# Optimization experiments

Measured on AMD Instinct MI355X. Metric: run time of the kernel, lower is better.

Reference implementation:

```python
import jax, jax.numpy as jnp
import numpy as np

E = 8      # num_experts
D = 1024   # input_size
H = 1024   # hidden_size
K = 2      # top_k
B = 2
S = 1024


def setup_inputs() -> dict:
    key = jax.random.key(0)
    ks = jax.random.split(key, 5)
    x = jax.random.normal(ks[0], (B, S, D), dtype=jnp.float32)
    p = jax.random.uniform(ks[1], (B * S, K), dtype=jnp.float32)
    expert_p = p / p.sum(axis=-1, keepdims=True)            # normalized top-k gates
    expert_idxs = jax.random.randint(ks[2], (B * S, K), 0, E)
    W1 = jax.random.normal(ks[3], (E, D, 2 * H), dtype=jnp.float32) * (D ** -0.5)
    W2 = jax.random.normal(ks[4], (E, H, D), dtype=jnp.float32) * (H ** -0.5)
    return {"x": x, "expert_p": expert_p, "expert_idxs": expert_idxs, "W1": W1, "W2": W2}


def reference(x, expert_p, expert_idxs, W1, W2):
    x_shape = x.shape
    xf = x.reshape(-1, x_shape[-1])                 # [N, D]
    n_tok = xf.shape[0]
    k = expert_idxs.shape[-1]
    x_pair = jnp.repeat(xf, k, axis=0)              # [N*K, D] token replicated per expert slot
    idx = expert_idxs.reshape(-1)                   # [N*K]
    p = expert_p.reshape(-1)                        # [N*K]
    y_pair = jnp.zeros((n_tok * k, x_shape[-1]), dtype=x.dtype)
    # loop over fixed small expert count; masked dense GEMM per expert
    for e in range(W1.shape[0]):
        m = (idx == e).astype(x.dtype)[:, None]     # [N*K, 1]
        hg = (x_pair * m) @ W1[e]                   # [N*K, 2H]
        h, g = jnp.split(hg, 2, axis=-1)            # chunk(2): (h, gates)
        a = jax.nn.silu(g) * h                      # SiLU-gated GLU
        y_pair = y_pair + (a @ W2[e]) * m           # [N*K, D]
    # combine: weight each pair by its gate prob and sum over top_k slots
    y = (y_pair * p[:, None]).reshape(n_tok, k, -1).sum(axis=1)
    return y.reshape(x_shape)
```

## Files before the change

kernel.cpp:

```cpp
#include <hip/hip_runtime.h>


typedef __bf16 bf16x8 __attribute__((ext_vector_type(8)));
typedef __bf16 bf16x4 __attribute__((ext_vector_type(4)));
typedef float  f32x4  __attribute__((ext_vector_type(4)));

#define NPAIR 4096
#define NTOK  2048
#define DDIM  1024
#define HDIM  1024
#define NEXP  8

#define ORDER_I   64
#define XB_OFF    (24576)
#define W1T_OFF   (XB_OFF + 4194304)
#define W2T_OFF   (W1T_OFF + 33554432)
#define ACT_OFF   (W2T_OFF + 16777216)

#define GLOAD_LDS16(g, l) \
    __builtin_amdgcn_global_load_lds( \
        (const __attribute__((address_space(1))) void*)(g), \
        (__attribute__((address_space(3))) void*)(l), 16, 0, 0)

__device__ __forceinline__ void tcvt64(const float* __restrict__ s,
                                       __bf16* __restrict__ d,
                                       int R, int C, int k0, int c0,
                                       float (*tt)[65], int tid) {
#pragma unroll
    for (int p = 0; p < 4; p++) {
        int kr = p * 16 + (tid >> 4);
        int nc = (tid & 15) * 4;
        *(float4*)&tt[kr][nc] = *(const float4*)(s + (size_t)(k0 + kr) * C + c0 + nc);
    }
    __syncthreads();
#pragma unroll
    for (int p = 0; p < 2; p++) {
        int cid = p * 256 + tid;
        int n = cid >> 3, kc = cid & 7;
        bf16x8 o;
#pragma unroll
        for (int j = 0; j < 8; j++) o[j] = (__bf16)tt[kc * 8 + j][n];
        *(bf16x8*)(d + (size_t)(c0 + n) * R + k0 + kc * 8) = o;
    }
}

__global__ __launch_bounds__(256) void prep_kernel(const float* __restrict__ x,
                                                   const float* __restrict__ W1,
                                                   const int* __restrict__ idx,
                                                   int* __restrict__ wsi,
                                                   __bf16* __restrict__ xb,
                                                   __bf16* __restrict__ w1t) {
    __shared__ float tt[64][65];
    __shared__ int cnt[NEXP];
    __shared__ int sbase, scur;
    const int b = blockIdx.x;
    const int tid = threadIdx.x;
    if (b < 4096) {
        int e = b >> 9, t2 = b & 511;
        int k0 = (t2 & 15) * 64, c0 = (t2 >> 4) * 64;
        tcvt64(W1 + (size_t)e * DDIM * 2 * HDIM, w1t + (size_t)e * 2 * HDIM * DDIM,
               DDIM, 2 * HDIM, k0, c0, tt, tid);
    } else if (b < 6144) {
        int i = (b - 4096) * 1024 + tid * 4;
        float4 v = *(const float4*)(x + i);
        bf16x4 o;
        o[0] = (__bf16)v.x; o[1] = (__bf16)v.y; o[2] = (__bf16)v.z; o[3] = (__bf16)v.w;
        *(bf16x4*)(xb + i) = o;
    } else {
        const int e = b - 6144;
        if (tid < NEXP) cnt[tid] = 0;
        if (tid == 0) scur = 0;
        __syncthreads();
        for (int i = tid; i < NPAIR; i += 256) atomicAdd(&cnt[idx[i] & 7], 1);
        __syncthreads();
        if (tid == 0) {
            int off = 0;
            for (int e2 = 0; e2 < NEXP; e2++) {
                if (e2 == e) { wsi[e] = cnt[e]; wsi[8 + e] = off; sbase = off; }
                off += (cnt[e2] + 127) & ~127;
            }
        }
        __syncthreads();
        for (int i = tid; i < NPAIR; i += 256) {
            if ((idx[i] & 7) == e) {
                int s = atomicAdd(&scur, 1);
                wsi[ORDER_I + sbase + s] = i;
            }
        }
    }
}

__global__ __launch_bounds__(256) void gemm1_kernel(const __bf16* __restrict__ xb,
                                                    const __bf16* __restrict__ w1t,
                                                    const int* __restrict__ wsi,
                                                    __bf16* __restrict__ act,
                                                    const float* __restrict__ W2,
                                                    __bf16* __restrict__ w2t,
                                                    float* __restrict__ out) {
    __shared__ __align__(16) char smem[24576];
    const int tid = threadIdx.x;
    const int z = blockIdx.z;

    if (z >= 8) {
        int aux = (z - 8) * 1024 + blockIdx.y * 16 + blockIdx.x;
        if (aux < 2048) {
            int e = aux >> 8, t2 = aux & 255;
            int k0 = (t2 & 15) * 64, c0 = (t2 >> 4) * 64;
            tcvt64(W2 + (size_t)e * HDIM * DDIM, w2t + (size_t)e * DDIM * HDIM,
                   HDIM, DDIM, k0, c0, (float (*)[65])smem, tid);
        } else if (aux < 2560) {
            int zb = aux - 2048;
            float4 z4 = {0.f, 0.f, 0.f, 0.f};
            int b4 = zb * 4096;
#pragma unroll
            for (int j = 0; j < 4; j++)
                *(float4*)(out + b4 + j * 1024 + tid * 4) = z4;
        }
        return;
    }

    const int e = z;
    const int cnt = wsi[e];
    const int m0 = blockIdx.y * 64;
    if (m0 >= cnt) return;
    const int base = wsi[8 + e];
    const int n0 = blockIdx.x * 64;
    const int* order = wsi + ORDER_I;
    const __bf16* w1e = w1t + (size_t)e * 2048 * 1024;

    __bf16 (*As)[64] = (__bf16 (*)[64])smem;
    __bf16 (*Bs)[64] = (__bf16 (*)[64])(smem + 8192);

    const int lane = tid & 63, w = tid >> 6;
    const int lm = lane & 15, q = lane >> 4;
    const int wm = w & 1, wn = w >> 1;
    const int x7 = lm & 7;
    const int sw0 = (q ^ x7) * 16;
    const int sw1 = ((4 + q) ^ x7) * 16;

    const __bf16* ga[2];
    const __bf16* gb[4];
#pragma unroll
    for (int j = 0; j < 2; j++) {
        int c = j * 256 + tid;
        int r = c >> 3;
        int ks = ((c & 7) ^ (r & 7)) * 8;
        int m = m0 + r; if (m >= cnt) m = cnt - 1;
        int tok = order[base + m] >> 1;
        ga[j] = xb + (size_t)tok * DDIM + ks;
    }
#pragma unroll
    for (int j = 0; j < 4; j++) {
        int c = j * 256 + tid;
        int r = c >> 3;
        int ks = ((c & 7) ^ (r & 7)) * 8;
        int half = r >> 6, rr = r & 63;
        int rb = (rr < 32) ? (n0 + half * 32 + rr)
                           : (HDIM + n0 + half * 32 + (rr - 32));
        gb[j] = w1e + (size_t)rb * DDIM + ks;
    }

    f32x4 acc[2][4];
#pragma unroll
    for (int mt = 0; mt < 2; mt++)
#pragma unroll
        for (int nt = 0; nt < 4; nt++) acc[mt][nt] = (f32x4){0.f, 0.f, 0.f, 0.f};

    for (int k0 = 0; k0 < DDIM; k0 += 64) {
        __syncthreads();
#pragma unroll
        for (int j = 0; j < 2; j++) {
            int c = j * 256 + tid;
            GLOAD_LDS16(ga[j], (char*)&As[0][0] + c * 16);
            ga[j] += 64;
        }
#pragma unroll
        for (int j = 0; j < 4; j++) {
            int c = j * 256 + tid;
            GLOAD_LDS16(gb[j], (char*)&Bs[0][0] + c * 16);
            gb[j] += 64;
        }
        __syncthreads();
#pragma unroll
        for (int kh = 0; kh < 2; kh++) {
            const int sw = kh ? sw1 : sw0;
            bf16x8 af[2];
#pragma unroll
            for (int mt = 0; mt < 2; mt++)
                af[mt] = *(const bf16x8*)((const char*)&As[wm * 32 + mt * 16 + lm][0] + sw);
#pragma unroll
            for (int nt = 0; nt < 4; nt++) {
                bf16x8 bfr = *(const bf16x8*)((const char*)&Bs[wn * 64 + nt * 16 + lm][0] + sw);
#pragma unroll
                for (int mt = 0; mt < 2; mt++)
                    acc[mt][nt] = __builtin_amdgcn_mfma_f32_16x16x32_bf16(af[mt], bfr, acc[mt][nt], 0, 0, 0);
            }
        }
    }

#pragma unroll
    for (int mt = 0; mt < 2; mt++) {
        int mbase = m0 + wm * 32 + mt * 16 + q * 4;
#pragma unroll
        for (int ntp = 0; ntp < 2; ntp++) {
            int col = n0 + wn * 32 + ntp * 16 + lm;
#pragma unroll
            for (int r = 0; r < 4; r++) {
                int m = mbase + r;
                if (m < cnt) {
                    float h = acc[mt][ntp][r];
                    float g = acc[mt][ntp + 2][r];
                    float a = h * (g / (1.f + __expf(-g)));
                    act[(size_t)(base + m) * HDIM + col] = (__bf16)a;
                }
            }
        }
    }
}

__global__ __launch_bounds__(256) void gemm2_kernel(const __bf16* __restrict__ act,
                                                    const __bf16* __restrict__ w2t,
                                                    const int* __restrict__ wsi,
                                                    const float* __restrict__ p,
                                                    float* __restrict__ out) {
    const int e = blockIdx.z;
    const int cnt = wsi[e];
    const int m0 = blockIdx.y * 64;
    if (m0 >= cnt) return;
    const int base = wsi[8 + e];
    const int n0 = blockIdx.x * 64;
    const int* order = wsi + ORDER_I;
    const __bf16* w2e = w2t + (size_t)e * 1024 * 1024;

    __shared__ __align__(16) __bf16 As[64][64];
    __shared__ __align__(16) __bf16 Bs[64][64];

    const int tid = threadIdx.x;
    const int lane = tid & 63, w = tid >> 6;
    const int lm = lane & 15, q = lane >> 4;
    const int wm = w & 1, wn = w >> 1;
    const int x7 = lm & 7;
    const int sw0 = (q ^ x7) * 16;
    const int sw1 = ((4 + q) ^ x7) * 16;

    const __bf16* ga[2];
    const __bf16* gb[2];
#pragma unroll
    for (int j = 0; j < 2; j++) {
        int c = j * 256 + tid;
        int r = c >> 3;
        int ks = ((c & 7) ^ (r & 7)) * 8;
        ga[j] = act + (size_t)(base + m0 + r) * HDIM + ks;
        gb[j] = w2e + (size_t)(n0 + r) * HDIM + ks;
    }

    f32x4 acc[2][2];
#pragma unroll
    for (int mt = 0; mt < 2; mt++)
#pragma unroll
        for (int nt = 0; nt < 2; nt++) acc[mt][nt] = (f32x4){0.f, 0.f, 0.f, 0.f};

    for (int k0 = 0; k0 < HDIM; k0 += 64) {
        __syncthreads();
#pragma unroll
        for (int j = 0; j < 2; j++) {
            int c = j * 256 + tid;
            GLOAD_LDS16(ga[j], (char*)&As[0][0] + c * 16);
            GLOAD_LDS16(gb[j], (char*)&Bs[0][0] + c * 16);
            ga[j] += 64; gb[j] += 64;
        }
        __syncthreads();
#pragma unroll
        for (int kh = 0; kh < 2; kh++) {
            const int sw = kh ? sw1 : sw0;
            bf16x8 af[2];
#pragma unroll
            for (int mt = 0; mt < 2; mt++)
                af[mt] = *(const bf16x8*)((const char*)&As[wm * 32 + mt * 16 + lm][0] + sw);
#pragma unroll
            for (int nt = 0; nt < 2; nt++) {
                bf16x8 bfr = *(const bf16x8*)((const char*)&Bs[wn * 32 + nt * 16 + lm][0] + sw);
#pragma unroll
                for (int mt = 0; mt < 2; mt++)
                    acc[mt][nt] = __builtin_amdgcn_mfma_f32_16x16x32_bf16(af[mt], bfr, acc[mt][nt], 0, 0, 0);
            }
        }
    }

    int pi[2][4];
    float pw[2][4];
#pragma unroll
    for (int mt = 0; mt < 2; mt++)
#pragma unroll
        for (int r = 0; r < 4; r++) {
            int gm = m0 + wm * 32 + mt * 16 + q * 4 + r;
            if (gm < cnt) {
                int pr = order[base + gm];
                pi[mt][r] = pr;
                pw[mt][r] = p[pr];
            } else pi[mt][r] = -1;
        }
#pragma unroll
    for (int mt = 0; mt < 2; mt++)
#pragma unroll
        for (int nt = 0; nt < 2; nt++) {
            int col = n0 + wn * 32 + nt * 16 + lm;
#pragma unroll
            for (int r = 0; r < 4; r++) {
                if (pi[mt][r] >= 0) {
                    int tok = pi[mt][r] >> 1;
                    atomicAdd(out + (size_t)tok * DDIM + col, pw[mt][r] * acc[mt][nt][r]);
                }
            }
        }
}

extern "C" void kernel_launch(void* const* d_in, const int* in_sizes, int n_in,
                              void* d_out, int out_size, void* d_ws, size_t ws_size,
                              hipStream_t stream) {
    (void)in_sizes; (void)n_in; (void)out_size; (void)ws_size;
    const float* x   = (const float*)d_in[0];
    const float* p   = (const float*)d_in[1];
    const int* eidx  = (const int*)d_in[2];
    const float* W1  = (const float*)d_in[3];
    const float* W2  = (const float*)d_in[4];
    float* out = (float*)d_out;

    char* ws = (char*)d_ws;
    int* wsi     = (int*)ws;
    __bf16* xb   = (__bf16*)(ws + XB_OFF);
    __bf16* w1t  = (__bf16*)(ws + W1T_OFF);
    __bf16* w2t  = (__bf16*)(ws + W2T_OFF);
    __bf16* act  = (__bf16*)(ws + ACT_OFF);

    prep_kernel<<<6152, 256, 0, stream>>>(x, W1, eidx, wsi, xb, w1t);
    gemm1_kernel<<<dim3(16, 64, 11), 256, 0, stream>>>(xb, w1t, wsi, act, W2, w2t, out);
    gemm2_kernel<<<dim3(16, 64, NEXP), 256, 0, stream>>>(act, w2t, wsi, p, out);
}
```

Baseline: 203.8 us.

## Drop weight transposes; read row-major bf16 weights via LDS transpose loads

Weight preparation now converts W1 and W2 to bf16 in their original row-major layout with plain vectorized copies, replacing the LDS-staged transpose-and-convert tiles. The GEMM kernels load K-major weight tiles into swizzled LDS and use ds_read_b64_tr_b16 to build the transposed MFMA B operands. Output zeroing moves into the prep kernel, and the auxiliary grid in gemm1 shrinks. This removes the costly strided transpose writes during prep, at the price of hand-written asm LDS reads with an explicit full lgkmcnt wait that may limit overlap.

```diff
diff --git a/kernel.cpp b/kernel.cpp
--- a/kernel.cpp
+++ b/kernel.cpp
@@ -4,6 +4,7 @@
 typedef __bf16 bf16x8 __attribute__((ext_vector_type(8)));
 typedef __bf16 bf16x4 __attribute__((ext_vector_type(4)));
 typedef float  f32x4  __attribute__((ext_vector_type(4)));
+typedef unsigned int u32x2 __attribute__((ext_vector_type(2)));
 
 #define NPAIR 4096
 #define NTOK  2048
@@ -13,35 +14,24 @@
 
 #define ORDER_I   64
 #define XB_OFF    (24576)
-#define W1T_OFF   (XB_OFF + 4194304)
-#define W2T_OFF   (W1T_OFF + 33554432)
-#define ACT_OFF   (W2T_OFF + 16777216)
+#define W1B_OFF   (XB_OFF + 4194304)
+#define W2B_OFF   (W1B_OFF + 33554432)
+#define ACT_OFF   (W2B_OFF + 16777216)
 
 #define GLOAD_LDS16(g, l) \
     __builtin_amdgcn_global_load_lds( \
         (const __attribute__((address_space(1))) void*)(g), \
         (__attribute__((address_space(3))) void*)(l), 16, 0, 0)
 
-__device__ __forceinline__ void tcvt64(const float* __restrict__ s,
-                                       __bf16* __restrict__ d,
-                                       int R, int C, int k0, int c0,
-                                       float (*tt)[65], int tid) {
-#pragma unroll
-    for (int p = 0; p < 4; p++) {
-        int kr = p * 16 + (tid >> 4);
-        int nc = (tid & 15) * 4;
-        *(float4*)&tt[kr][nc] = *(const float4*)(s + (size_t)(k0 + kr) * C + c0 + nc);
-    }
-    __syncthreads();
-#pragma unroll
-    for (int p = 0; p < 2; p++) {
-        int cid = p * 256 + tid;
-        int n = cid >> 3, kc = cid & 7;
-        bf16x8 o;
-#pragma unroll
-        for (int j = 0; j < 8; j++) o[j] = (__bf16)tt[kc * 8 + j][n];
-        *(bf16x8*)(d + (size_t)(c0 + n) * R + k0 + kc * 8) = o;
-    }
+#define LDS_OFF(p) ((unsigned int)(unsigned long long)(__attribute__((address_space(3))) void*)(p))
+
+__device__ __forceinline__ void cvt8(const float* __restrict__ s, __bf16* __restrict__ d) {
+    float4 v0 = *(const float4*)s;
+    float4 v1 = *(const float4*)(s + 4);
+    bf16x8 o;
+    o[0] = (__bf16)v0.x; o[1] = (__bf16)v0.y; o[2] = (__bf16)v0.z; o[3] = (__bf16)v0.w;
+    o[4] = (__bf16)v1.x; o[5] = (__bf16)v1.y; o[6] = (__bf16)v1.z; o[7] = (__bf16)v1.w;
+    *(bf16x8*)d = o;
 }
 
 __global__ __launch_bounds__(256) void prep_kernel(const float* __restrict__ x,
@@ -49,25 +39,30 @@
                                                    const int* __restrict__ idx,
                                                    int* __restrict__ wsi,
                                                    __bf16* __restrict__ xb,
-                                                   __bf16* __restrict__ w1t) {
-    __shared__ float tt[64][65];
+                                                   __bf16* __restrict__ w1b,
+                                                   float* __restrict__ out) {
     __shared__ int cnt[NEXP];
     __shared__ int sbase, scur;
     const int b = blockIdx.x;
     const int tid = threadIdx.x;
-    if (b < 4096) {
-        int e = b >> 9, t2 = b & 511;
-        int k0 = (t2 & 15) * 64, c0 = (t2 >> 4) * 64;
-        tcvt64(W1 + (size_t)e * DDIM * 2 * HDIM, w1t + (size_t)e * 2 * HDIM * DDIM,
-               DDIM, 2 * HDIM, k0, c0, tt, tid);
-    } else if (b < 6144) {
-        int i = (b - 4096) * 1024 + tid * 4;
-        float4 v = *(const float4*)(x + i);
-        bf16x4 o;
-        o[0] = (__bf16)v.x; o[1] = (__bf16)v.y; o[2] = (__bf16)v.z; o[3] = (__bf16)v.w;
-        *(bf16x4*)(xb + i) = o;
+    if (b < 2048) {
+        size_t base = (size_t)b * 8192 + tid * 8;
+#pragma unroll
+        for (int j = 0; j < 4; j++)
+            cvt8(W1 + base + j * 2048, w1b + base + j * 2048);
+    } else if (b < 2560) {
+        size_t base = (size_t)(b - 2048) * 4096 + tid * 8;
+#pragma unroll
+        for (int j = 0; j < 2; j++)
+            cvt8(x + base + j * 2048, xb + base + j * 2048);
+    } else if (b < 3072) {
+        float4 z4 = {0.f, 0.f, 0.f, 0.f};
+        size_t base = (size_t)(b - 2560) * 4096 + tid * 4;
+#pragma unroll
+        for (int j = 0; j < 4; j++)
+            *(float4*)(out + base + j * 1024) = z4;
     } else {
-        const int e = b - 6144;
+        const int e = b - 3072;
         if (tid < NEXP) cnt[tid] = 0;
         if (tid == 0) scur = 0;
         __syncthreads();
@@ -91,31 +86,21 @@
 }
 
 __global__ __launch_bounds__(256) void gemm1_kernel(const __bf16* __restrict__ xb,
-                                                    const __bf16* __restrict__ w1t,
+                                                    const __bf16* __restrict__ w1b,
                                                     const int* __restrict__ wsi,
                                                     __bf16* __restrict__ act,
                                                     const float* __restrict__ W2,
-                                                    __bf16* __restrict__ w2t,
-                                                    float* __restrict__ out) {
+                                                    __bf16* __restrict__ w2b) {
     __shared__ __align__(16) char smem[24576];
     const int tid = threadIdx.x;
     const int z = blockIdx.z;
 
     if (z >= 8) {
-        int aux = (z - 8) * 1024 + blockIdx.y * 16 + blockIdx.x;
-        if (aux < 2048) {
-            int e = aux >> 8, t2 = aux & 255;
-            int k0 = (t2 & 15) * 64, c0 = (t2 >> 4) * 64;
-            tcvt64(W2 + (size_t)e * HDIM * DDIM, w2t + (size_t)e * DDIM * HDIM,
-                   HDIM, DDIM, k0, c0, (float (*)[65])smem, tid);
-        } else if (aux < 2560) {
-            int zb = aux - 2048;
-            float4 z4 = {0.f, 0.f, 0.f, 0.f};
-            int b4 = zb * 4096;
-#pragma unroll
-            for (int j = 0; j < 4; j++)
-                *(float4*)(out + b4 + j * 1024 + tid * 4) = z4;
-        }
+        int aux = blockIdx.y * 16 + blockIdx.x;
+        size_t base = (size_t)aux * 8192 + tid * 8;
+#pragma unroll
+        for (int j = 0; j < 4; j++)
+            cvt8(W2 + base + j * 2048, w2b + base + j * 2048);
         return;
     }
 
@@ -126,10 +111,10 @@
     const int base = wsi[8 + e];
     const int n0 = blockIdx.x * 64;
     const int* order = wsi + ORDER_I;
-    const __bf16* w1e = w1t + (size_t)e * 2048 * 1024;
+    const __bf16* w1e = w1b + (size_t)e * 2048 * 1024;
 
     __bf16 (*As)[64] = (__bf16 (*)[64])smem;
-    __bf16 (*Bs)[64] = (__bf16 (*)[64])(smem + 8192);
+    __bf16* Bs = (__bf16*)(smem + 8192);
 
     const int lane = tid & 63, w = tid >> 6;
     const int lm = lane & 15, q = lane >> 4;
@@ -139,26 +124,38 @@
     const int sw1 = ((4 + q) ^ x7) * 16;
 
     const __bf16* ga[2];
-    const __bf16* gb[4];
 #pragma unroll
     for (int j = 0; j < 2; j++) {
         int c = j * 256 + tid;
-        int r = c >> 3;
-        int ks = ((c & 7) ^ (r & 7)) * 8;
-        int m = m0 + r; if (m >= cnt) m = cnt - 1;
+        int r2 = c >> 3;
+        int ks = ((c & 7) ^ (r2 & 7)) * 8;
+        int m = m0 + r2; if (m >= cnt) m = cnt - 1;
         int tok = order[base + m] >> 1;
         ga[j] = xb + (size_t)tok * DDIM + ks;
     }
+    const __bf16* gb[4];
 #pragma unroll
     for (int j = 0; j < 4; j++) {
         int c = j * 256 + tid;
-        int r = c >> 3;
-        int ks = ((c & 7) ^ (r & 7)) * 8;
-        int half = r >> 6, rr = r & 63;
-        int rb = (rr < 32) ? (n0 + half * 32 + rr)
-                           : (HDIM + n0 + half * 32 + (rr - 32));
-        gb[j] = w1e + (size_t)rb * DDIM + ks;
-    }
+        int k = c >> 4;
+        int ul = (c & 15) ^ ((k & 7) << 1);
+        int u7 = ul & 7, h64 = ul >> 3;
+        int colW = (u7 < 4) ? (n0 + h64 * 32 + u7 * 8)
+                            : (HDIM + n0 + h64 * 32 + (u7 - 4) * 8);
+        gb[j] = w1e + (size_t)k * 2048 + colW;
+    }
+
+    const int r = lm;
+    unsigned int trb[4][2];
+#pragma unroll
+    for (int nt = 0; nt < 4; nt++)
+#pragma unroll
+        for (int pr = 0; pr < 2; pr++) {
+            int row = q * 8 + pr * 4 + (r >> 2);
+            int ul = wn * 8 + nt * 2 + ((r & 3) >> 1);
+            int up = ul ^ (((pr * 4 + (r >> 2)) & 7) << 1);
+            trb[nt][pr] = LDS_OFF(Bs) + row * 256 + up * 16 + (r & 1) * 8;
+        }
 
     f32x4 acc[2][4];
 #pragma unroll
@@ -170,15 +167,13 @@
         __syncthreads();
 #pragma unroll
         for (int j = 0; j < 2; j++) {
-            int c = j * 256 + tid;
-            GLOAD_LDS16(ga[j], (char*)&As[0][0] + c * 16);
+            GLOAD_LDS16(ga[j], (char*)smem + (j * 256 + tid) * 16);
             ga[j] += 64;
         }
 #pragma unroll
         for (int j = 0; j < 4; j++) {
-            int c = j * 256 + tid;
-            GLOAD_LDS16(gb[j], (char*)&Bs[0][0] + c * 16);
-            gb[j] += 64;
+            GLOAD_LDS16(gb[j], (char*)Bs + (j * 256 + tid) * 16);
+            gb[j] += 64 * 2048;
         }
         __syncthreads();
 #pragma unroll
@@ -188,12 +183,24 @@
 #pragma unroll
             for (int mt = 0; mt < 2; mt++)
                 af[mt] = *(const bf16x8*)((const char*)&As[wm * 32 + mt * 16 + lm][0] + sw);
+            u32x2 t0[4], t1[4];
 #pragma unroll
             for (int nt = 0; nt < 4; nt++) {
-                bf16x8 bfr = *(const bf16x8*)((const char*)&Bs[wn * 64 + nt * 16 + lm][0] + sw);
+                asm volatile("ds_read_b64_tr_b16 %0, %1 offset:%c2"
+                             : "=&v"(t0[nt]) : "v"(trb[nt][0]), "i"(kh * 8192));
+                asm volatile("ds_read_b64_tr_b16 %0, %1 offset:%c2"
+                             : "=&v"(t1[nt]) : "v"(trb[nt][1]), "i"(kh * 8192));
+            }
+            asm volatile("s_waitcnt lgkmcnt(0)" ::: "memory");
+            __builtin_amdgcn_sched_barrier(0);
+#pragma unroll
+            for (int nt = 0; nt < 4; nt++) {
+                union { unsigned int u[4]; bf16x8 v; } bb;
+                bb.u[0] = t0[nt][0]; bb.u[1] = t0[nt][1];
+                bb.u[2] = t1[nt][0]; bb.u[3] = t1[nt][1];
 #pragma unroll
                 for (int mt = 0; mt < 2; mt++)
-                    acc[mt][nt] = __builtin_amdgcn_mfma_f32_16x16x32_bf16(af[mt], bfr, acc[mt][nt], 0, 0, 0);
+                    acc[mt][nt] = __builtin_amdgcn_mfma_f32_16x16x32_bf16(af[mt], bb.v, acc[mt][nt], 0, 0, 0);
             }
         }
     }
@@ -205,11 +212,11 @@
         for (int ntp = 0; ntp < 2; ntp++) {
             int col = n0 + wn * 32 + ntp * 16 + lm;
 #pragma unroll
-            for (int r = 0; r < 4; r++) {
-                int m = mbase + r;
+            for (int rr = 0; rr < 4; rr++) {
+                int m = mbase + rr;
                 if (m < cnt) {
-                    float h = acc[mt][ntp][r];
-                    float g = acc[mt][ntp + 2][r];
+                    float h = acc[mt][ntp][rr];
+                    float g = acc[mt][ntp + 2][rr];
                     float a = h * (g / (1.f + __expf(-g)));
                     act[(size_t)(base + m) * HDIM + col] = (__bf16)a;
                 }
@@ -219,7 +226,7 @@
 }
 
 __global__ __launch_bounds__(256) void gemm2_kernel(const __bf16* __restrict__ act,
-                                                    const __bf16* __restrict__ w2t,
+                                                    const __bf16* __restrict__ w2b,
                                                     const int* __restrict__ wsi,
                                                     const float* __restrict__ p,
                                                     float* __restrict__ out) {
@@ -230,10 +237,11 @@
     const int base = wsi[8 + e];
     const int n0 = blockIdx.x * 64;
     const int* order = wsi + ORDER_I;
-    const __bf16* w2e = w2t + (size_t)e * 1024 * 1024;
-
-    __shared__ __align__(16) __bf16 As[64][64];
-    __shared__ __align__(16) __bf16 Bs[64][64];
+    const __bf16* w2e = w2b + (size_t)e * 1024 * 1024;
+
+    __shared__ __align__(16) char smem[16384];
+    __bf16 (*As)[64] = (__bf16 (*)[64])smem;
+    __bf16* Bs = (__bf16*)(smem + 8192);
 
     const int tid = threadIdx.x;
     const int lane = tid & 63, w = tid >> 6;
@@ -244,14 +252,30 @@
     const int sw1 = ((4 + q) ^ x7) * 16;
 
     const __bf16* ga[2];
-    const __bf16* gb[2];
 #pragma unroll
     for (int j = 0; j < 2; j++) {
         int c = j * 256 + tid;
-        int r = c >> 3;
-        int ks = ((c & 7) ^ (r & 7)) * 8;
-        ga[j] = act + (size_t)(base + m0 + r) * HDIM + ks;
-        gb[j] = w2e + (size_t)(n0 + r) * HDIM + ks;
+        int r2 = c >> 3;
+        int ks = ((c & 7) ^ (r2 & 7)) * 8;
+        ga[j] = act + (size_t)(base + m0 + r2) * HDIM + ks;
+    }
+    const __bf16* gb[2];
+#pragma unroll
+    for (int j = 0; j < 2; j++) {
+        int c = j * 256 + tid;
+        int k = c >> 3;
+        int ul = (c & 7) ^ ((k & 3) << 1);
+        gb[j] = w2e + (size_t)k * 1024 + n0 + ul * 8;
+    }
+
+    const int r = lm;
+    unsigned int trb[2];
+#pragma unroll
+    for (int nt = 0; nt < 2; nt++) {
+        int row = q * 8 + (r >> 2);
+        int ul = wn * 4 + nt * 2 + ((r & 3) >> 1);
+        int up = ul ^ (((r >> 2) & 3) << 1);
+        trb[nt] = LDS_OFF(Bs) + row * 128 + up * 16 + (r & 1) * 8;
     }
 
     f32x4 acc[2][2];
@@ -264,10 +288,9 @@
         __syncthreads();
 #pragma unroll
         for (int j = 0; j < 2; j++) {
-            int c = j * 256 + tid;
-            GLOAD_LDS16(ga[j], (char*)&As[0][0] + c * 16);
-            GLOAD_LDS16(gb[j], (char*)&Bs[0][0] + c * 16);
-            ga[j] += 64; gb[j] += 64;
+            GLOAD_LDS16(ga[j], (char*)smem + (j * 256 + tid) * 16);
+            GLOAD_LDS16(gb[j], (char*)Bs + (j * 256 + tid) * 16);
+            ga[j] += 64; gb[j] += 64 * 1024;
         }
         __syncthreads();
 #pragma unroll
@@ -277,12 +300,24 @@
 #pragma unroll
             for (int mt = 0; mt < 2; mt++)
                 af[mt] = *(const bf16x8*)((const char*)&As[wm * 32 + mt * 16 + lm][0] + sw);
+            u32x2 t0[2], t1[2];
 #pragma unroll
             for (int nt = 0; nt < 2; nt++) {
-                bf16x8 bfr = *(const bf16x8*)((const char*)&Bs[wn * 32 + nt * 16 + lm][0] + sw);
+                asm volatile("ds_read_b64_tr_b16 %0, %1 offset:%c2"
+                             : "=&v"(t0[nt]) : "v"(trb[nt]), "i"(kh * 4096));
+                asm volatile("ds_read_b64_tr_b16 %0, %1 offset:%c2"
+                             : "=&v"(t1[nt]) : "v"(trb[nt]), "i"(kh * 4096 + 512));
+            }
+            asm volatile("s_waitcnt lgkmcnt(0)" ::: "memory");
+            __builtin_amdgcn_sched_barrier(0);
+#pragma unroll
+            for (int nt = 0; nt < 2; nt++) {
+                union { unsigned int u[4]; bf16x8 v; } bb;
+                bb.u[0] = t0[nt][0]; bb.u[1] = t0[nt][1];
+                bb.u[2] = t1[nt][0]; bb.u[3] = t1[nt][1];
 #pragma unroll
                 for (int mt = 0; mt < 2; mt++)
-                    acc[mt][nt] = __builtin_amdgcn_mfma_f32_16x16x32_bf16(af[mt], bfr, acc[mt][nt], 0, 0, 0);
+                    acc[mt][nt] = __builtin_amdgcn_mfma_f32_16x16x32_bf16(af[mt], bb.v, acc[mt][nt], 0, 0, 0);
             }
         }
     }
@@ -292,13 +327,13 @@
 #pragma unroll
     for (int mt = 0; mt < 2; mt++)
 #pragma unroll
-        for (int r = 0; r < 4; r++) {
-            int gm = m0 + wm * 32 + mt * 16 + q * 4 + r;
+        for (int rr = 0; rr < 4; rr++) {
+            int gm = m0 + wm * 32 + mt * 16 + q * 4 + rr;
             if (gm < cnt) {
                 int pr = order[base + gm];
-                pi[mt][r] = pr;
-                pw[mt][r] = p[pr];
-            } else pi[mt][r] = -1;
+                pi[mt][rr] = pr;
+                pw[mt][rr] = p[pr];
+            } else pi[mt][rr] = -1;
         }
 #pragma unroll
     for (int mt = 0; mt < 2; mt++)
@@ -306,10 +341,10 @@
         for (int nt = 0; nt < 2; nt++) {
             int col = n0 + wn * 32 + nt * 16 + lm;
 #pragma unroll
-            for (int r = 0; r < 4; r++) {
-                if (pi[mt][r] >= 0) {
-                    int tok = pi[mt][r] >> 1;
-                    atomicAdd(out + (size_t)tok * DDIM + col, pw[mt][r] * acc[mt][nt][r]);
+            for (int rr = 0; rr < 4; rr++) {
+                if (pi[mt][rr] >= 0) {
+                    int tok = pi[mt][rr] >> 1;
+                    atomicAdd(out + (size_t)tok * DDIM + col, pw[mt][rr] * acc[mt][nt][rr]);
                 }
             }
         }
@@ -329,11 +364,11 @@
     char* ws = (char*)d_ws;
     int* wsi     = (int*)ws;
     __bf16* xb   = (__bf16*)(ws + XB_OFF);
-    __bf16* w1t  = (__bf16*)(ws + W1T_OFF);
-    __bf16* w2t  = (__bf16*)(ws + W2T_OFF);
+    __bf16* w1b  = (__bf16*)(ws + W1B_OFF);
+    __bf16* w2b  = (__bf16*)(ws + W2B_OFF);
     __bf16* act  = (__bf16*)(ws + ACT_OFF);
 
-    prep_kernel<<<6152, 256, 0, stream>>>(x, W1, eidx, wsi, xb, w1t);
-    gemm1_kernel<<<dim3(16, 64, 11), 256, 0, stream>>>(xb, w1t, wsi, act, W2, w2t, out);
-    gemm2_kernel<<<dim3(16, 64, NEXP), 256, 0, stream>>>(act, w2t, wsi, p, out);
-}
+    prep_kernel<<<3080, 256, 0, stream>>>(x, W1, eidx, wsi, xb, w1b, out);
+    gemm1_kernel<<<dim3(16, 64, 9), 256, 0, stream>>>(xb, w1b, wsi, act, W2, w2b);
+    gemm2_kernel<<<dim3(16, 64, NEXP), 256, 0, stream>>>(act, w2b, wsi, p, out);
+}
```

Result: slower. 214.9 us (+5.5%).

## Double-buffer LDS tiles in both expert GEMMs to overlap loads with MFMA

Applied to the files above, without the earlier changes.

Both grouped GEMM kernels now prefetch the next K-slice into a second LDS buffer with direct global-to-LDS loads while MFMAs run on the current buffer. Each step ends with one waitcnt plus barrier instead of two syncthreads. s_setprio is raised around the MFMA block to favour math issue. This doubles LDS use per block (48KB in gemm1, 32KB in gemm2), which may reduce occupancy, and it relies on the sched_barrier to keep the prefetch ahead of the LDS reads.

```diff
diff --git a/kernel.cpp b/kernel.cpp
--- a/kernel.cpp
+++ b/kernel.cpp
@@ -97,7 +97,7 @@
                                                     const float* __restrict__ W2,
                                                     __bf16* __restrict__ w2t,
                                                     float* __restrict__ out) {
-    __shared__ __align__(16) char smem[24576];
+    __shared__ __align__(16) char smem[49152];
     const int tid = threadIdx.x;
     const int z = blockIdx.z;
 
@@ -128,9 +128,6 @@
     const int* order = wsi + ORDER_I;
     const __bf16* w1e = w1t + (size_t)e * 2048 * 1024;
 
-    __bf16 (*As)[64] = (__bf16 (*)[64])smem;
-    __bf16 (*Bs)[64] = (__bf16 (*)[64])(smem + 8192);
-
     const int lane = tid & 63, w = tid >> 6;
     const int lm = lane & 15, q = lane >> 4;
     const int wm = w & 1, wn = w >> 1;
@@ -166,21 +163,37 @@
 #pragma unroll
         for (int nt = 0; nt < 4; nt++) acc[mt][nt] = (f32x4){0.f, 0.f, 0.f, 0.f};
 
-    for (int k0 = 0; k0 < DDIM; k0 += 64) {
-        __syncthreads();
-#pragma unroll
-        for (int j = 0; j < 2; j++) {
-            int c = j * 256 + tid;
-            GLOAD_LDS16(ga[j], (char*)&As[0][0] + c * 16);
-            ga[j] += 64;
-        }
-#pragma unroll
-        for (int j = 0; j < 4; j++) {
-            int c = j * 256 + tid;
-            GLOAD_LDS16(gb[j], (char*)&Bs[0][0] + c * 16);
-            gb[j] += 64;
-        }
-        __syncthreads();
+#pragma unroll
+    for (int j = 0; j < 2; j++) {
+        GLOAD_LDS16(ga[j], smem + (j * 256 + tid) * 16);
+        ga[j] += 64;
+    }
+#pragma unroll
+    for (int j = 0; j < 4; j++) {
+        GLOAD_LDS16(gb[j], smem + 8192 + (j * 256 + tid) * 16);
+        gb[j] += 64;
+    }
+    asm volatile("s_waitcnt vmcnt(0)" ::: "memory");
+    __builtin_amdgcn_s_barrier();
+
+    for (int t = 0; t < 16; ++t) {
+        char* cbase = smem + (t & 1) * 24576;
+        if (t < 15) {
+            char* nbase = smem + ((t & 1) ^ 1) * 24576;
+#pragma unroll
+            for (int j = 0; j < 2; j++) {
+                GLOAD_LDS16(ga[j], nbase + (j * 256 + tid) * 16);
+                ga[j] += 64;
+            }
+#pragma unroll
+            for (int j = 0; j < 4; j++) {
+                GLOAD_LDS16(gb[j], nbase + 8192 + (j * 256 + tid) * 16);
+                gb[j] += 64;
+            }
+        }
+        __builtin_amdgcn_sched_barrier(0);
+        __bf16 (*As)[64] = (__bf16 (*)[64])cbase;
+        __bf16 (*Bs)[64] = (__bf16 (*)[64])(cbase + 8192);
 #pragma unroll
         for (int kh = 0; kh < 2; kh++) {
             const int sw = kh ? sw1 : sw0;
@@ -188,6 +201,7 @@
 #pragma unroll
             for (int mt = 0; mt < 2; mt++)
                 af[mt] = *(const bf16x8*)((const char*)&As[wm * 32 + mt * 16 + lm][0] + sw);
+            __builtin_amdgcn_s_setprio(1);
 #pragma unroll
             for (int nt = 0; nt < 4; nt++) {
                 bf16x8 bfr = *(const bf16x8*)((const char*)&Bs[wn * 64 + nt * 16 + lm][0] + sw);
@@ -195,7 +209,10 @@
                 for (int mt = 0; mt < 2; mt++)
                     acc[mt][nt] = __builtin_amdgcn_mfma_f32_16x16x32_bf16(af[mt], bfr, acc[mt][nt], 0, 0, 0);
             }
-        }
+            __builtin_amdgcn_s_setprio(0);
+        }
+        asm volatile("s_waitcnt vmcnt(0)" ::: "memory");
+        __builtin_amdgcn_s_barrier();
     }
 
 #pragma unroll
@@ -232,8 +249,7 @@
     const int* order = wsi + ORDER_I;
     const __bf16* w2e = w2t + (size_t)e * 1024 * 1024;
 
-    __shared__ __align__(16) __bf16 As[64][64];
-    __shared__ __align__(16) __bf16 Bs[64][64];
+    __shared__ __align__(16) char smem[32768];
 
     const int tid = threadIdx.x;
     const int lane = tid & 63, w = tid >> 6;
@@ -260,16 +276,29 @@
 #pragma unroll
         for (int nt = 0; nt < 2; nt++) acc[mt][nt] = (f32x4){0.f, 0.f, 0.f, 0.f};
 
-    for (int k0 = 0; k0 < HDIM; k0 += 64) {
-        __syncthreads();
-#pragma unroll
-        for (int j = 0; j < 2; j++) {
-            int c = j * 256 + tid;
-            GLOAD_LDS16(ga[j], (char*)&As[0][0] + c * 16);
-            GLOAD_LDS16(gb[j], (char*)&Bs[0][0] + c * 16);
-            ga[j] += 64; gb[j] += 64;
-        }
-        __syncthreads();
+#pragma unroll
+    for (int j = 0; j < 2; j++) {
+        GLOAD_LDS16(ga[j], smem + (j * 256 + tid) * 16);
+        GLOAD_LDS16(gb[j], smem + 8192 + (j * 256 + tid) * 16);
+        ga[j] += 64; gb[j] += 64;
+    }
+    asm volatile("s_waitcnt vmcnt(0)" ::: "memory");
+    __builtin_amdgcn_s_barrier();
+
+    for (int t = 0; t < 16; ++t) {
+        char* cbase = smem + (t & 1) * 16384;
+        if (t < 15) {
+            char* nbase = smem + ((t & 1) ^ 1) * 16384;
+#pragma unroll
+            for (int j = 0; j < 2; j++) {
+                GLOAD_LDS16(ga[j], nbase + (j * 256 + tid) * 16);
+                GLOAD_LDS16(gb[j], nbase + 8192 + (j * 256 + tid) * 16);
+                ga[j] += 64; gb[j] += 64;
+            }
+        }
+        __builtin_amdgcn_sched_barrier(0);
+        __bf16 (*As)[64] = (__bf16 (*)[64])cbase;
+        __bf16 (*Bs)[64] = (__bf16 (*)[64])(cbase + 8192);
 #pragma unroll
         for (int kh = 0; kh < 2; kh++) {
             const int sw = kh ? sw1 : sw0;
@@ -277,6 +306,7 @@
 #pragma unroll
             for (int mt = 0; mt < 2; mt++)
                 af[mt] = *(const bf16x8*)((const char*)&As[wm * 32 + mt * 16 + lm][0] + sw);
+            __builtin_amdgcn_s_setprio(1);
 #pragma unroll
             for (int nt = 0; nt < 2; nt++) {
                 bf16x8 bfr = *(const bf16x8*)((const char*)&Bs[wn * 32 + nt * 16 + lm][0] + sw);
@@ -284,7 +314,10 @@
                 for (int mt = 0; mt < 2; mt++)
                     acc[mt][nt] = __builtin_amdgcn_mfma_f32_16x16x32_bf16(af[mt], bfr, acc[mt][nt], 0, 0, 0);
             }
-        }
+            __builtin_amdgcn_s_setprio(0);
+        }
+        asm volatile("s_waitcnt vmcnt(0)" ::: "memory");
+        __builtin_amdgcn_s_barrier();
     }
 
     int pi[2][4];
```

New measurement: 206.6 us. Within noise of the previous version (+1.4%).
